# Performance work log

Hardware: AMD Instinct MI355X
Metric: run time of the kernel (lower is better)

## Reference

```python
import jax, jax.numpy as jnp
import numpy as np

B, S_SRC, D, H, DH, FF, L, V, W, NG = 2, 4093, 768, 12, 64, 3072, 2, 50265, 256, 3
S = S_SRC + NG            # 4096, multiple of one-sided window W=256
NC = S // W               # 16 chunks
EPS = 1e-5
CLS_IDS = (50261, 50262, 50263)
NEG = -1e9


def setup_inputs() -> dict:
    key = jax.random.key(0)
    ks = jax.random.split(key, 16)
    std = 0.02
    inp = {
        "src": jax.random.randint(ks[0], (B, S_SRC), 0, 50260),
        "mask_src": jnp.ones((B, S_SRC), dtype=bool),
        "cluster_sizes": jax.random.randint(ks[1], (B,), 0, 16),
        "word_emb": jax.random.normal(ks[2], (V, D), jnp.float32) * std,
        "pos_emb": jax.random.normal(ks[3], (S, D), jnp.float32) * std,
        "emb_ln": jnp.stack([jnp.ones((D,)), jnp.zeros((D,))]),              # [2,D] scale,bias
        "attn_w": jax.random.normal(ks[4], (L, 7, D, D), jnp.float32) * std,  # q,k,v,qg,kg,vg,o
        "attn_b": jnp.zeros((L, 7, D), jnp.float32),
        "ln_p": jnp.stack([jnp.stack([jnp.ones((D,)), jnp.zeros((D,)), jnp.ones((D,)), jnp.zeros((D,))]) for _ in range(L)]),  # [L,4,D]
        "ffn_w1": jax.random.normal(ks[5], (L, D, FF), jnp.float32) * std,
        "ffn_b1": jnp.zeros((L, FF), jnp.float32),
        "ffn_w2": jax.random.normal(ks[6], (L, FF, D), jnp.float32) * std,
        "ffn_b2": jnp.zeros((L, D), jnp.float32),
        "cls_w": jax.random.normal(ks[7], (3, D), jnp.float32) * std,
        "cls_b": jnp.zeros((3,), jnp.float32),
    }
    return inp


def _ln(x, scale, bias):
    mu = jnp.mean(x, axis=-1, keepdims=True)
    var = jnp.mean(jnp.square(x - mu), axis=-1, keepdims=True)
    return (x - mu) * jax.lax.rsqrt(var + EPS) * scale + bias


def _encoder(ids, mask, word_emb, pos_emb, emb_ln, attn_w, attn_b, ln_p,
             ffn_w1, ffn_b1, ffn_w2, ffn_b2):
    x = _ln(word_emb[ids] + pos_emb[None, :S], emb_ln[0], emb_ln[1])  # [B,S,D]

    # static banded-attention index structure (chunk of W queries sees 3W keys)
    idx = np.arange(NC)[:, None] * W + np.arange(3 * W)[None, :]  # into padded seq
    kp = idx - W                                                   # absolute key pos
    valid = (kp >= 0) & (kp < S)
    kpc = jnp.asarray(np.clip(kp, 0, S - 1))
    qpos = np.arange(W)[:, None]
    band = jnp.asarray(np.abs(np.arange(3 * W)[None, :] - W - qpos) <= W)  # [W,3W]
    # global & padding keys removed from windowed attention (HF semantics)
    keymask = mask[:, kpc] & jnp.asarray(valid)[None] & jnp.asarray(kp >= NG)[None]  # [B,NC,3W]
    allowed = band[None, None] & keymask[:, :, None, :]  # [B,NC,W,3W]
    scale = 1.0 / np.sqrt(DH)

    def layer(x, p):
        aw, ab, lnp, w1, b1, w2, b2 = p
        def proj(i):
            return (x @ aw[i] + ab[i]).reshape(B, S, H, DH).transpose(0, 2, 1, 3)
        q = proj(0) * scale
        k = proj(1)
        v = proj(2)
        kpad = jnp.pad(k, ((0, 0), (0, 0), (W, W), (0, 0)))
        vpad = jnp.pad(v, ((0, 0), (0, 0), (W, W), (0, 0)))
        Kc = kpad[:, :, kpc + W]  # [B,H,NC,3W,DH] (kpc+W indexes padded)
        Vc = vpad[:, :, kpc + W]
        qc = q.reshape(B, H, NC, W, DH)
        s_loc = jnp.einsum('bhcqd,bhckd->bhcqk', qc, Kc)
        s_loc = jnp.where(allowed[:, None], s_loc, NEG)
        s_glb = jnp.einsum('bhcqd,bhgd->bhcqg', qc, k[:, :, :NG])  # all tokens -> global keys
        probs = jax.nn.softmax(jnp.concatenate([s_glb, s_loc], axis=-1), axis=-1)
        out = (jnp.einsum('bhcqg,bhgd->bhcqd', probs[..., :NG], v[:, :, :NG])
               + jnp.einsum('bhcqk,bhckd->bhcqd', probs[..., NG:], Vc))
        out = out.reshape(B, H, S, DH)
        # global query rows: full attention with global q/k/v projections
        qg = ((x[:, :NG] @ aw[3] + ab[3]).reshape(B, NG, H, DH)) * scale
        kg = (x @ aw[4] + ab[4]).reshape(B, S, H, DH)
        vg = (x @ aw[5] + ab[5]).reshape(B, S, H, DH)
        sg = jnp.einsum('bghd,bshd->bhgs', qg, kg)
        sg = jnp.where(mask[:, None, None, :], sg, NEG)
        og = jnp.einsum('bhgs,bshd->bhgd', jax.nn.softmax(sg, axis=-1), vg)
        out = out.at[:, :, :NG, :].set(og)
        out = out.transpose(0, 2, 1, 3).reshape(B, S, D)
        xa = _ln(x + out @ aw[6] + ab[6], lnp[0], lnp[1])
        h = jax.nn.gelu(xa @ w1 + b1, approximate=False)
        return _ln(xa + h @ w2 + b2, lnp[2], lnp[3]), None

    x, _ = jax.lax.scan(layer, x, (attn_w, attn_b, ln_p, ffn_w1, ffn_b1, ffn_w2, ffn_b2))
    return x


def reference(src, mask_src, cluster_sizes, word_emb, pos_emb, emb_ln, attn_w,
              attn_b, ln_p, ffn_w1, ffn_b1, ffn_w2, ffn_b2, cls_w, cls_b):
    ids = jnp.concatenate([jnp.broadcast_to(jnp.asarray(CLS_IDS), (B, NG)), src], axis=1)
    mask = jnp.concatenate([jnp.ones((B, NG), dtype=bool), mask_src], axis=1)
    h = _encoder(ids, mask, word_emb, pos_emb, emb_ln, attn_w, attn_b, ln_p,
                 ffn_w1, ffn_b1, ffn_w2, ffn_b2)  # [B,S,D]
    mf = mask.astype(h.dtype)
    scores = [jax.nn.sigmoid(h[:, i] @ cls_w[i] + cls_b[i]) * mf[:, i] for i in range(3)]
    verd, pros, cons = (s[:, None] for s in scores)
    return verd, pros, cons, mf[:, 0][:, None]
```

## Files before the change

### kernel.cpp

```cpp
#include <hip/hip_runtime.h>
#include <hip/hip_bf16.h>
#include <math.h>

#define B_    2
#define SSRC_ 4093
#define D_    768
#define H_    12
#define DH_   64
#define FF_   3072
#define NG_   3
#define W_    256
#define S_    4096
#define NC_   16
#define NSPLIT_ 16
#define QB_   128

typedef __attribute__((ext_vector_type(8))) short frag_ab;
typedef __attribute__((ext_vector_type(4))) float f32x4;

#define GL16(gp, lp) __builtin_amdgcn_global_load_lds( \
    (const __attribute__((address_space(1))) void*)(gp), \
    (__attribute__((address_space(3))) void*)(lp), 16, 0, 0)

__device__ __forceinline__ float bflo(unsigned int w) {
    union { float f; unsigned int i; } c; c.i = w << 16; return c.f;
}
__device__ __forceinline__ float bfhi(unsigned int w) {
    union { float f; unsigned int i; } c; c.i = w & 0xffff0000u; return c.f;
}
__device__ __forceinline__ void unp8(uint4 t, float* o) {
    o[0] = bflo(t.x); o[1] = bfhi(t.x); o[2] = bflo(t.y); o[3] = bfhi(t.y);
    o[4] = bflo(t.z); o[5] = bfhi(t.z); o[6] = bflo(t.w); o[7] = bfhi(t.w);
}
__device__ __forceinline__ unsigned short f2bfu(float x) {
    __hip_bfloat16 h = __float2bfloat16(x);
    return *reinterpret_cast<unsigned short*>(&h);
}

__device__ __forceinline__ float block_sum(float v, float* red) {
    int tid = threadIdx.x;
    red[tid] = v;
    __syncthreads();
#pragma unroll
    for (int off = 128; off >= 1; off >>= 1) {
        if (tid < off) red[tid] += red[tid + off];
        __syncthreads();
    }
    float r = red[0];
    __syncthreads();
    return r;
}

__device__ __forceinline__ float block_max(float v, float* red) {
    int tid = threadIdx.x;
    red[tid] = v;
    __syncthreads();
#pragma unroll
    for (int off = 128; off >= 1; off >>= 1) {
        if (tid < off) red[tid] = fmaxf(red[tid], red[tid + off]);
        __syncthreads();
    }
    float r = red[0];
    __syncthreads();
    return r;
}

__device__ __forceinline__ void storeO(float* p, float v) { *p = v; }
__device__ __forceinline__ void storeO(__hip_bfloat16* p, float v) { *p = __float2bfloat16(v); }

__global__ __launch_bounds__(256) void embed_ln_k(
    const int* __restrict__ src, const float* __restrict__ we,
    const float* __restrict__ pe, const float* __restrict__ gam,
    const float* __restrict__ bet, float* __restrict__ X,
    __hip_bfloat16* __restrict__ Xb) {
    __shared__ float red[256];
    int row = blockIdx.x;
    int b = row >> 12;
    int s = row & (S_ - 1);
    int tid = threadIdx.x;
    int id = (s < NG_) ? (50261 + s) : src[b * SSRC_ + (s - NG_)];
    const float* wr = we + (size_t)id * D_;
    const float* pr = pe + (size_t)s * D_;
    float v[3];
    float lsum = 0.f;
#pragma unroll
    for (int j = 0; j < 3; ++j) {
        int c = tid + j * 256;
        v[j] = wr[c] + pr[c];
        lsum += v[j];
    }
    float mu = block_sum(lsum, red) * (1.0f / 768.0f);
    float ls2 = 0.f;
#pragma unroll
    for (int j = 0; j < 3; ++j) { float d = v[j] - mu; ls2 += d * d; }
    float var = block_sum(ls2, red) * (1.0f / 768.0f);
    float rs = rsqrtf(var + 1e-5f);
    float* xr = X + (size_t)row * D_;
    __hip_bfloat16* xbr = Xb + (size_t)row * D_;
#pragma unroll
    for (int j = 0; j < 3; ++j) {
        int c = tid + j * 256;
        float o = (v[j] - mu) * rs * gam[c] + bet[c];
        xr[c] = o;
        xbr[c] = __float2bfloat16(o);
    }
}

__global__ __launch_bounds__(256) void residual_ln_k(
    const float* __restrict__ x, const float* __restrict__ y,
    const float* __restrict__ y2, const float* __restrict__ gam,
    const float* __restrict__ bet, float* __restrict__ out,
    __hip_bfloat16* __restrict__ outb) {
    __shared__ float red[256];
    int row = blockIdx.x;
    int tid = threadIdx.x;
    const float* xr = x + (size_t)row * D_;
    const float* yr = y + (size_t)row * D_;
    const float* y2r = y2 ? y2 + (size_t)row * D_ : nullptr;
    float v[3];
    float lsum = 0.f;
#pragma unroll
    for (int j = 0; j < 3; ++j) {
        int c = tid + j * 256;
        v[j] = xr[c] + yr[c];
        if (y2r) v[j] += y2r[c];
        lsum += v[j];
    }
    float mu = block_sum(lsum, red) * (1.0f / 768.0f);
    float ls2 = 0.f;
#pragma unroll
    for (int j = 0; j < 3; ++j) { float d = v[j] - mu; ls2 += d * d; }
    float var = block_sum(ls2, red) * (1.0f / 768.0f);
    float rs = rsqrtf(var + 1e-5f);
    float* orow = out + (size_t)row * D_;
    __hip_bfloat16* obr = outb ? outb + (size_t)row * D_ : nullptr;
#pragma unroll
    for (int j = 0; j < 3; ++j) {
        int c = tid + j * 256;
        float o = (v[j] - mu) * rs * gam[c] + bet[c];
        orow[c] = o;
        if (obr) obr[c] = __float2bfloat16(o);
    }
}

__global__ __launch_bounds__(256) void convt_k(
    const float* __restrict__ W, __hip_bfloat16* __restrict__ WT,
    int K, int N, int npb ) {
    __shared__ float tile[32][33];
    int mat = blockIdx.x / npb;
    int bx = blockIdx.x - mat * npb;
    int by = blockIdx.y;
    const float* Wm = W + (size_t)mat * K * N;
    __hip_bfloat16* WTm = WT + (size_t)mat * N * K;
    int tx = threadIdx.x & 31, ty = threadIdx.x >> 5;
#pragma unroll
    for (int i = 0; i < 32; i += 8)
        tile[ty + i][tx] = Wm[(size_t)(by * 32 + ty + i) * N + bx * 32 + tx];
    __syncthreads();
#pragma unroll
    for (int i = 0; i < 32; i += 8)
        WTm[(size_t)(bx * 32 + ty + i) * K + by * 32 + tx] = __float2bfloat16(tile[tx][ty + i]);
}

__global__ void pack_bias_k(const float* __restrict__ ab, float* __restrict__ dst) {
    int j = blockIdx.x * 256 + threadIdx.x;
    if (j >= 5 * 768) return;
    int mat = j / 768, c = j - mat * 768;
    int i = (mat < 3) ? mat : mat + 1;
    dst[j] = ab[i * 768 + c];
}

template <int EPI, int SPLIT>
__global__ __launch_bounds__(256) void mfma_gemm_k(
    const __hip_bfloat16* __restrict__ A, const __hip_bfloat16* __restrict__ BT,
    const float* __restrict__ bias, void* __restrict__ Cout,
    int M, int N, int K, size_t matstride) {
    __shared__ __align__(16) __hip_bfloat16 As[4096];
    __shared__ __align__(16) __hip_bfloat16 Bs[4096];
    int tid = threadIdx.x;
    int lane = tid & 63;
    int w = tid >> 6, wr = w >> 1, wc = w & 1;
    int brow = blockIdx.y * 128, bcol = blockIdx.x * 128;
    int z = blockIdx.z, nz = gridDim.z;
    int Kz = K / nz;
    int r0 = tid >> 2, k0 = (tid & 3) * 8;
    const __hip_bfloat16* Ag0 = A + (size_t)(brow + r0) * K + z * Kz + k0;
    const __hip_bfloat16* Ag1 = Ag0 + (size_t)64 * K;
    const __hip_bfloat16* Bg0 = BT + (size_t)(bcol + r0) * K + z * Kz + k0;
    const __hip_bfloat16* Bg1 = Bg0 + (size_t)64 * K;
    __hip_bfloat16* lA0 = &As[tid * 8];
    __hip_bfloat16* lA1 = &As[tid * 8 + 2048];
    __hip_bfloat16* lB0 = &Bs[tid * 8];
    __hip_bfloat16* lB1 = &Bs[tid * 8 + 2048];

    f32x4 acc[4][4];
#pragma unroll
    for (int m = 0; m < 4; ++m)
#pragma unroll
        for (int n = 0; n < 4; ++n) acc[m][n] = (f32x4){0.f, 0.f, 0.f, 0.f};

    int l15 = lane & 15, kb = lane >> 4;
    int aoff = (wr * 64 + l15) * 32 + kb * 8;
    int boff = (wc * 64 + l15) * 32 + kb * 8;

    for (int kt = 0; kt < Kz; kt += 32) {
        GL16(Ag0 + kt, lA0);
        GL16(Ag1 + kt, lA1);
        GL16(Bg0 + kt, lB0);
        GL16(Bg1 + kt, lB1);
        __syncthreads();
        frag_ab af[4], bf[4];
#pragma unroll
        for (int m = 0; m < 4; ++m) af[m] = *(const frag_ab*)&As[aoff + m * 512];
#pragma unroll
        for (int n = 0; n < 4; ++n) bf[n] = *(const frag_ab*)&Bs[boff + n * 512];
        __builtin_amdgcn_s_setprio(1);
#pragma unroll
        for (int m = 0; m < 4; ++m)
#pragma unroll
            for (int n = 0; n < 4; ++n)
                acc[m][n] = __builtin_amdgcn_mfma_f32_16x16x32_bf16(af[m], bf[n], acc[m][n], 0, 0, 0);
        __builtin_amdgcn_s_setprio(0);
        __syncthreads();
    }

    size_t zoff = (size_t)z * M * N;
#pragma unroll
    for (int m = 0; m < 4; ++m) {
        int rowb = brow + wr * 64 + m * 16 + (lane >> 4) * 4;
#pragma unroll
        for (int n = 0; n < 4; ++n) {
            int col = bcol + wc * 64 + n * 16 + l15;
            float bv = (z == 0) ? bias[col] : 0.f;
#pragma unroll
            for (int r = 0; r < 4; ++r) {
                float v = acc[m][n][r] + bv;
                size_t idx;
                if (SPLIT) {
                    int mat = col / 768;
                    idx = (size_t)mat * matstride + (size_t)(rowb + r) * 768 + (col - mat * 768);
                } else {
                    idx = zoff + (size_t)(rowb + r) * N + col;
                }
                if (EPI == 0) {
                    ((float*)Cout)[idx] = v;
                } else if (EPI == 1) {
                    ((__hip_bfloat16*)Cout)[idx] = __float2bfloat16(v);
                } else {
                    float g = 0.5f * v * (1.0f + erff(v * 0.70710678118654752f));
                    ((__hip_bfloat16*)Cout)[idx] = __float2bfloat16(g);
                }
            }
        }
    }
}

__global__ __launch_bounds__(256) void skinny_gemm_k(
    const float* __restrict__ A, const float* __restrict__ W,
    float* __restrict__ partial, int N, int K) {
    __shared__ float Asl[6][64];
    __shared__ float red[4][6][64];
    int tid = threadIdx.x;
    int cl = tid & 63;
    int kg = tid >> 6;
    int col = blockIdx.x * 64 + cl;
    int k0 = blockIdx.y * 64;
    for (int i = tid; i < 6 * 64; i += 256)
        Asl[i >> 6][i & 63] = A[(size_t)(i >> 6) * K + k0 + (i & 63)];
    __syncthreads();
    float acc[6] = {0.f, 0.f, 0.f, 0.f, 0.f, 0.f};
#pragma unroll
    for (int kk = 0; kk < 16; ++kk) {
        int k = kg * 16 + kk;
        float wv = W[(size_t)(k0 + k) * N + col];
#pragma unroll
        for (int m = 0; m < 6; ++m) acc[m] += Asl[m][k] * wv;
    }
#pragma unroll
    for (int m = 0; m < 6; ++m) red[kg][m][cl] = acc[m];
    __syncthreads();
    for (int i = tid; i < 6 * 64; i += 256) {
        int m = i >> 6, lane = i & 63;
        float s = red[0][m][lane] + red[1][m][lane] + red[2][m][lane] + red[3][m][lane];
        partial[(size_t)blockIdx.y * 6 * N + (size_t)m * N + blockIdx.x * 64 + lane] = s;
    }
}

__global__ __launch_bounds__(256) void skinny_reduce_k(
    const float* __restrict__ partial, const float* __restrict__ bias,
    float* __restrict__ outp, int N, int KS, int gelu) {
    int idx = blockIdx.x * 256 + threadIdx.x;
    if (idx >= 6 * N) return;
    int m = idx / N, col = idx - m * N;
    float s = bias[col];
    for (int kb = 0; kb < KS; ++kb)
        s += partial[(size_t)kb * 6 * N + (size_t)m * N + col];
    if (gelu) s = 0.5f * s * (1.0f + erff(s * 0.70710678118654752f));
    outp[(size_t)m * N + col] = s;
}

__global__ __launch_bounds__(256, 1) void local_attn_k(
    const __hip_bfloat16* __restrict__ Q, const __hip_bfloat16* __restrict__ K,
    const __hip_bfloat16* __restrict__ V, __hip_bfloat16* __restrict__ O) {
    __shared__ __align__(16) __hip_bfloat16 K_lds[64 * 72];
    __shared__ __align__(16) __hip_bfloat16 VT_lds[64 * 72];
    __shared__ __align__(16) __hip_bfloat16 P_lds[4][16 * 72];

    const int cq = blockIdx.x, h = blockIdx.y, b = blockIdx.z;
    const int tid = threadIdx.x;
    const int lane = tid & 63;
    const int w = tid >> 6;
    const int l15 = lane & 15, g4 = lane >> 4;
    const int cbase = cq * QB_;

    frag_ab qf[2][2];
#pragma unroll
    for (int qt = 0; qt < 2; ++qt) {
        int qa = cbase + w * 32 + qt * 16 + l15;
        const __hip_bfloat16* qp = Q + (size_t)(b * S_ + qa) * D_ + h * DH_ + g4 * 8;
        qf[qt][0] = *(const frag_ab*)qp;
        qf[qt][1] = *(const frag_ab*)(qp + 32);
    }

    f32x4 o[2][4];
#pragma unroll
    for (int qt = 0; qt < 2; ++qt)
#pragma unroll
        for (int dt = 0; dt < 4; ++dt) o[qt][dt] = (f32x4){0.f, 0.f, 0.f, 0.f};
    float mrun[2] = {-1e30f, -1e30f};
    float lrun[2] = {0.f, 0.f};

    int kw0 = cbase - W_; if (kw0 < 0) kw0 = 0;
    int kw1 = cbase + QB_ + W_; if (kw1 > S_) kw1 = S_;
    int ntiles = (kw1 - kw0) >> 6;

    char* Pw = (char*)P_lds[w];

    for (int t = 0; t < ntiles; ++t) {
        int k0 = kw0 + t * 64;
        __syncthreads();
        {
            const __hip_bfloat16* Kg = K + (size_t)(b * S_ + k0) * D_ + h * DH_;
            const __hip_bfloat16* Vg = V + (size_t)(b * S_ + k0) * D_ + h * DH_;
#pragma unroll
            for (int it = 0; it < 2; ++it) {
                int idx = tid + it * 256;
                int kk = idx >> 3, d0 = (idx & 7) * 8;
                uint4 kv = *(const uint4*)(Kg + (size_t)kk * D_ + d0);
                *(uint4*)&K_lds[kk * 72 + d0] = kv;
                uint4 vv = *(const uint4*)(Vg + (size_t)kk * D_ + d0);
                unsigned short vs[8];
                *(uint4*)vs = vv;
#pragma unroll
                for (int j = 0; j < 8; ++j) {
                    int dd = d0 + j;
                    int boff = dd * 144 + ((kk * 2) ^ (((dd >> 3) & 7) << 4));
                    *(unsigned short*)((char*)VT_lds + boff) = vs[j];
                }
            }
        }
        __syncthreads();

        frag_ab kf[4][2];
#pragma unroll
        for (int kt = 0; kt < 4; ++kt) {
            const char* kp = (const char*)K_lds + (kt * 16 + l15) * 144 + g4 * 16;
            kf[kt][0] = *(const frag_ab*)kp;
            kf[kt][1] = *(const frag_ab*)(kp + 64);
        }
        frag_ab vf[4][2];
#pragma unroll
        for (int dt = 0; dt < 4; ++dt) {
            int drow = dt * 16 + l15;
            int swz = ((drow >> 3) & 7) << 4;
            const char* vp = (const char*)VT_lds + drow * 144;
            vf[dt][0] = *(const frag_ab*)(vp + ((g4 * 16) ^ swz));
            vf[dt][1] = *(const frag_ab*)(vp + ((g4 * 16 + 64) ^ swz));
        }

#pragma unroll
        for (int qt = 0; qt < 2; ++qt) {
            f32x4 st[4];
            __builtin_amdgcn_s_setprio(1);
#pragma unroll
            for (int kt = 0; kt < 4; ++kt) {
                f32x4 z = (f32x4){0.f, 0.f, 0.f, 0.f};
                z = __builtin_amdgcn_mfma_f32_16x16x32_bf16(kf[kt][0], qf[qt][0], z, 0, 0, 0);
                z = __builtin_amdgcn_mfma_f32_16x16x32_bf16(kf[kt][1], qf[qt][1], z, 0, 0, 0);
                st[kt] = z;
            }
            __builtin_amdgcn_s_setprio(0);
            int qa = cbase + w * 32 + qt * 16 + l15;
            float sv[16];
            float mx = -1e30f;
#pragma unroll
            for (int kt = 0; kt < 4; ++kt)
#pragma unroll
                for (int r = 0; r < 4; ++r) {
                    int ka = k0 + kt * 16 + g4 * 4 + r;
                    float s = st[kt][r] * 0.125f;
                    bool bad = (ka < NG_) | (ka - qa > W_) | (qa - ka > W_);
                    s = bad ? -1e30f : s;
                    sv[kt * 4 + r] = s;
                    mx = fmaxf(mx, s);
                }
            mx = fmaxf(mx, __shfl_xor(mx, 16));
            mx = fmaxf(mx, __shfl_xor(mx, 32));
            float mnew = fmaxf(fmaxf(mrun[qt], mx), -60.0f);
            if (__any(mnew != mrun[qt])) {
                float fsc = __expf(mrun[qt] - mnew);
                mrun[qt] = mnew;
#pragma unroll
                for (int dt = 0; dt < 4; ++dt) o[qt][dt] *= fsc;
                lrun[qt] *= fsc;
            }
            float psum = 0.f;
            unsigned short pb[16];
#pragma unroll
            for (int i = 0; i < 16; ++i) {
                float p = __expf(sv[i] - mrun[qt]);
                psum += p;
                pb[i] = f2bfu(p);
            }
            psum += __shfl_xor(psum, 16);
            psum += __shfl_xor(psum, 32);
            lrun[qt] += psum;
#pragma unroll
            for (int kt = 0; kt < 4; ++kt)
#pragma unroll
                for (int rp = 0; rp < 2; ++rp) {
                    unsigned vpk = (unsigned)pb[kt * 4 + rp * 2] | ((unsigned)pb[kt * 4 + rp * 2 + 1] << 16);
                    int kloc = kt * 16 + g4 * 4 + rp * 2;
                    *(unsigned*)(Pw + l15 * 144 + kloc * 2) = vpk;
                }
            frag_ab pf0 = *(const frag_ab*)(Pw + l15 * 144 + g4 * 16);
            frag_ab pf1 = *(const frag_ab*)(Pw + l15 * 144 + g4 * 16 + 64);
            __builtin_amdgcn_s_setprio(1);
#pragma unroll
            for (int dt = 0; dt < 4; ++dt) {
                o[qt][dt] = __builtin_amdgcn_mfma_f32_16x16x32_bf16(vf[dt][0], pf0, o[qt][dt], 0, 0, 0);
                o[qt][dt] = __builtin_amdgcn_mfma_f32_16x16x32_bf16(vf[dt][1], pf1, o[qt][dt], 0, 0, 0);
            }
            __builtin_amdgcn_s_setprio(0);
        }
    }

    uint4 kgc[3][2];
    uint2 vgd[3][4];
#pragma unroll
    for (int gk = 0; gk < NG_; ++gk) {
        const __hip_bfloat16* kp = K + (size_t)(b * S_ + gk) * D_ + h * DH_ + g4 * 8;
        kgc[gk][0] = *(const uint4*)kp;
        kgc[gk][1] = *(const uint4*)(kp + 32);
        const __hip_bfloat16* vp = V + (size_t)(b * S_ + gk) * D_ + h * DH_ + g4 * 4;
#pragma unroll
        for (int dt = 0; dt < 4; ++dt)
            vgd[gk][dt] = *(const uint2*)(vp + dt * 16);
    }
#pragma unroll
    for (int qt = 0; qt < 2; ++qt) {
        float sg[3];
#pragma unroll
        for (int gk = 0; gk < NG_; ++gk) {
            float part = 0.f;
#pragma unroll
            for (int s = 0; s < 2; ++s) {
                uint4 qw = *(uint4*)&qf[qt][s];
                uint4 kw = kgc[gk][s];
                part += bflo(qw.x) * bflo(kw.x) + bfhi(qw.x) * bfhi(kw.x);
                part += bflo(qw.y) * bflo(kw.y) + bfhi(qw.y) * bfhi(kw.y);
                part += bflo(qw.z) * bflo(kw.z) + bfhi(qw.z) * bfhi(kw.z);
                part += bflo(qw.w) * bflo(kw.w) + bfhi(qw.w) * bfhi(kw.w);
            }
            part += __shfl_xor(part, 16);
            part += __shfl_xor(part, 32);
            sg[gk] = part * 0.125f;
        }
        float mx3 = fmaxf(fmaxf(sg[0], sg[1]), sg[2]);
        float mnew = fmaxf(fmaxf(mrun[qt], mx3), -60.0f);
        float fsc = __expf(mrun[qt] - mnew);
        mrun[qt] = mnew;
#pragma unroll
        for (int dt = 0; dt < 4; ++dt) o[qt][dt] *= fsc;
        lrun[qt] *= fsc;
        float pg[3];
        float psum = 0.f;
#pragma unroll
        for (int gk = 0; gk < NG_; ++gk) { pg[gk] = __expf(sg[gk] - mnew); psum += pg[gk]; }
        lrun[qt] += psum;
#pragma unroll
        for (int dt = 0; dt < 4; ++dt) {
#pragma unroll
            for (int gk = 0; gk < NG_; ++gk) {
                uint2 vv = vgd[gk][dt];
                o[qt][dt][0] += pg[gk] * bflo(vv.x);
                o[qt][dt][1] += pg[gk] * bfhi(vv.x);
                o[qt][dt][2] += pg[gk] * bflo(vv.y);
                o[qt][dt][3] += pg[gk] * bfhi(vv.y);
            }
        }
    }

#pragma unroll
    for (int qt = 0; qt < 2; ++qt) {
        float linv = 1.0f / lrun[qt];
        int qa = cbase + w * 32 + qt * 16 + l15;
        __hip_bfloat16* orow = O + (size_t)(b * S_ + qa) * D_ + h * DH_;
#pragma unroll
        for (int dt = 0; dt < 4; ++dt) {
            unsigned short pk[4];
#pragma unroll
            for (int r = 0; r < 4; ++r) pk[r] = f2bfu(o[qt][dt][r] * linv);
            *(uint2*)(orow + dt * 16 + g4 * 4) = *(uint2*)pk;
        }
    }
}

__global__ __launch_bounds__(256) void gattn_part_k(
    const float* __restrict__ qg, const __hip_bfloat16* __restrict__ KG,
    const __hip_bfloat16* __restrict__ VG, float* __restrict__ gpart) {
    __shared__ float sc[256];
    __shared__ float qs[DH_];
    __shared__ float red[256];
    __shared__ float rv[16][64];
    int split = blockIdx.x;
    int gh = blockIdx.y;
    int g = gh / H_, h = gh - g * H_;
    int b = blockIdx.z;
    int tid = threadIdx.x;
    if (tid < DH_) qs[tid] = qg[(size_t)(b * NG_ + g) * D_ + h * DH_ + tid] * 0.125f;
    __syncthreads();
    int s0 = split * (S_ / NSPLIT_);
    float acc = 0.f;
    {
        const __hip_bfloat16* kp = KG + (size_t)(b * S_ + s0 + tid) * D_ + h * DH_;
#pragma unroll
        for (int c8 = 0; c8 < 8; ++c8) {
            uint4 t = *(const uint4*)(kp + c8 * 8);
            float f[8]; unp8(t, f);
#pragma unroll
            for (int j = 0; j < 8; ++j) acc += qs[c8 * 8 + j] * f[j];
        }
    }
    float m = block_max(acc, red);
    float e = __expf(acc - m);
    sc[tid] = e;
    float l = block_sum(e, red);
    int sgq = tid >> 4, dq = (tid & 15) * 4;
    float a0 = 0.f, a1 = 0.f, a2 = 0.f, a3 = 0.f;
    const __hip_bfloat16* vbase = VG + (size_t)(b * S_ + s0 + sgq * 16) * D_ + h * DH_ + dq;
#pragma unroll
    for (int i = 0; i < 16; ++i) {
        float p = sc[sgq * 16 + i];
        uint2 vv = *(const uint2*)(vbase + (size_t)i * D_);
        a0 += p * bflo(vv.x); a1 += p * bfhi(vv.x);
        a2 += p * bflo(vv.y); a3 += p * bfhi(vv.y);
    }
    rv[sgq][dq] = a0; rv[sgq][dq + 1] = a1; rv[sgq][dq + 2] = a2; rv[sgq][dq + 3] = a3;
    __syncthreads();
    float* op = gpart + ((size_t)((b * NG_ + g) * H_ + h) * NSPLIT_ + split) * 66;
    if (tid == 0) { op[0] = m; op[1] = l; }
    if (tid < DH_) {
        float s = 0.f;
#pragma unroll
        for (int j = 0; j < 16; ++j) s += rv[j][tid];
        op[2 + tid] = s;
    }
}

template <typename TO>
__global__ __launch_bounds__(64) void gattn_comb_k(
    const float* __restrict__ gpart, TO* __restrict__ outp, int rowStride) {
    int g = blockIdx.x, h = blockIdx.y, b = blockIdx.z;
    int tid = threadIdx.x;
    const float* base = gpart + (size_t)((b * NG_ + g) * H_ + h) * NSPLIT_ * 66;
    float M = -1e30f;
#pragma unroll
    for (int p = 0; p < NSPLIT_; ++p) M = fmaxf(M, base[p * 66]);
    float l = 0.f, o = 0.f;
#pragma unroll
    for (int p = 0; p < NSPLIT_; ++p) {
        float wgt = __expf(base[p * 66] - M);
        l += wgt * base[p * 66 + 1];
        o += wgt * base[p * 66 + 2 + tid];
    }
    storeO(&outp[(size_t)(b * rowStride + g) * D_ + h * DH_ + tid], o / l);
}

__global__ void gather6_k(const float* __restrict__ X, float* __restrict__ xg) {
    int r = blockIdx.x;
    int b = r / NG_, g = r % NG_;
    for (int c = threadIdx.x; c < D_; c += blockDim.x)
        xg[(size_t)r * D_ + c] = X[(size_t)(b * S_ + g) * D_ + c];
}

__global__ __launch_bounds__(256) void classifier_k(
    const float* __restrict__ x26, const float* __restrict__ cw,
    const float* __restrict__ cb, float* __restrict__ out) {
    __shared__ float red[256];
    int tid = threadIdx.x;
    for (int i = 0; i < 3; ++i) {
        for (int b = 0; b < B_; ++b) {
            const float* xr = x26 + (size_t)(b * NG_ + i) * D_;
            const float* wr = cw + (size_t)i * D_;
            float p = 0.f;
            for (int c = tid; c < D_; c += 256) p += xr[c] * wr[c];
            float dotv = block_sum(p, red);
            if (tid == 0) out[i * B_ + b] = 1.0f / (1.0f + __expf(-(dotv + cb[i])));
        }
    }
    if (tid == 0) { out[6] = 1.0f; out[7] = 1.0f; }
}

extern "C" void kernel_launch(void* const* d_in, const int* in_sizes, int n_in,
                              void* d_out, int out_size, void* d_ws, size_t ws_size,
                              hipStream_t stream) {
    const int*   src      = (const int*)d_in[0];
    const float* word_emb = (const float*)d_in[3];
    const float* pos_emb  = (const float*)d_in[4];
    const float* emb_ln   = (const float*)d_in[5];
    const float* attn_w   = (const float*)d_in[6];
    const float* attn_b   = (const float*)d_in[7];
    const float* ln_p     = (const float*)d_in[8];
    const float* ffn_w1   = (const float*)d_in[9];
    const float* ffn_b1   = (const float*)d_in[10];
    const float* ffn_w2   = (const float*)d_in[11];
    const float* ffn_b2   = (const float*)d_in[12];
    const float* cls_w    = (const float*)d_in[13];
    const float* cls_b    = (const float*)d_in[14];
    float* out = (float*)d_out;

    const size_t NT = (size_t)B_ * S_ * D_;
    float* base = (float*)d_ws;
    float* X  = base;
    float* P4 = base + NT;
    __hip_bfloat16* Xb  = (__hip_bfloat16*)(base + 2 * NT);
    __hip_bfloat16* Qb  = (__hip_bfloat16*)(base + 5 * NT / 2);
    __hip_bfloat16* Kb  = (__hip_bfloat16*)(base + 3 * NT);
    __hip_bfloat16* Vb  = (__hip_bfloat16*)(base + 7 * NT / 2);
    __hip_bfloat16* KGb = (__hip_bfloat16*)(base + 4 * NT);
    __hip_bfloat16* VGb = (__hip_bfloat16*)(base + 9 * NT / 2);
    __hip_bfloat16* AOb = (__hip_bfloat16*)(base + 5 * NT);
    __hip_bfloat16* HCb = (__hip_bfloat16*)(base + 11 * NT / 2);
    float* pj1 = base + 15 * NT / 2;
    float* pj2 = base + 17 * NT / 2;
    __hip_bfloat16* wq5 = (__hip_bfloat16*)(base + 19 * NT / 2);
    __hip_bfloat16* wo  = wq5 + 5 * 589824;
    __hip_bfloat16* wg1 = wo + 589824;
    __hip_bfloat16* wf1 = wg1 + 2 * 589824;
    __hip_bfloat16* wf2 = wf1 + 2359296;
    float* SM  = (float*)(wf2 + 2359296);
    float* xg  = SM;
    float* qg6 = xg + 6 * D_;
    float* og6 = qg6 + 6 * D_;
    float* pr6 = og6 + 6 * D_;
    float* xa6 = pr6 + 6 * D_;
    float* h6  = xa6 + 6 * D_;
    float* f6  = h6 + 6 * FF_;
    float* x26 = f6 + 6 * D_;
    float* bias5 = x26 + 6 * D_;
    float* part = bias5 + 5 * D_;
    float* gpart = part;

    const int M = B_ * S_;
    dim3 blk(256);

    auto aw = [&](int l, int i) { return attn_w + ((size_t)(l * 7 + i)) * D_ * D_; };
    auto ab = [&](int l, int i) { return attn_b + (size_t)(l * 7 + i) * D_; };
    auto lnp = [&](int l, int i) { return ln_p + (size_t)(l * 4 + i) * D_; };

    auto skinny = [&](const float* A6, const float* Wm, const float* bias,
                      float* out6, int N, int K, int gelu) {
        skinny_gemm_k<<<dim3(N / 64, K / 64), blk, 0, stream>>>(A6, Wm, part, N, K);
        skinny_reduce_k<<<dim3((6 * N + 255) / 256), blk, 0, stream>>>(part, bias, out6, N, K / 64, gelu);
    };

    embed_ln_k<<<M, blk, 0, stream>>>(src, word_emb, pos_emb, emb_ln, emb_ln + D_, X, Xb);

    convt_k<<<dim3(24 * 3, 24), blk, 0, stream>>>(aw(0, 0), wq5, D_, D_, 24);
    convt_k<<<dim3(24 * 2, 24), blk, 0, stream>>>(aw(0, 4), wq5 + 3 * 589824, D_, D_, 24);
    pack_bias_k<<<15, blk, 0, stream>>>(ab(0, 0), bias5);
    mfma_gemm_k<1, 1><<<dim3(3840 / 128, 64), blk, 0, stream>>>(Xb, wq5, bias5, Qb, M, 3840, D_, NT);
    local_attn_k<<<dim3(S_ / QB_, H_, B_), blk, 0, stream>>>(Qb, Kb, Vb, AOb);
    gather6_k<<<B_ * NG_, blk, 0, stream>>>(X, xg);
    skinny(xg, aw(0, 3), ab(0, 3), qg6, D_, D_, 0);
    gattn_part_k<<<dim3(NSPLIT_, NG_ * H_, B_), blk, 0, stream>>>(qg6, KGb, VGb, gpart);
    gattn_comb_k<__hip_bfloat16><<<dim3(NG_, H_, B_), dim3(64), 0, stream>>>(gpart, AOb, S_);
    convt_k<<<dim3(24, 24), blk, 0, stream>>>(aw(0, 6), wo, D_, D_, 24);
    mfma_gemm_k<0, 0><<<dim3(6, 64, 2), blk, 0, stream>>>(AOb, wo, ab(0, 6), pj1, M, D_, D_, 0);
    residual_ln_k<<<M, blk, 0, stream>>>(X, pj1, pj2, lnp(0, 0), lnp(0, 1), P4, Xb);
    convt_k<<<dim3(96, 24), blk, 0, stream>>>(ffn_w1, wf1, D_, FF_, 96);
    convt_k<<<dim3(24, 96), blk, 0, stream>>>(ffn_w2, wf2, FF_, D_, 24);
    mfma_gemm_k<2, 0><<<dim3(24, 64), blk, 0, stream>>>(Xb, wf1, ffn_b1, HCb, M, FF_, D_, 0);
    mfma_gemm_k<0, 0><<<dim3(6, 64, 2), blk, 0, stream>>>(HCb, wf2, ffn_b2, pj1, M, D_, FF_, 0);
    residual_ln_k<<<M, blk, 0, stream>>>(P4, pj1, pj2, lnp(0, 2), lnp(0, 3), X, Xb);

    convt_k<<<dim3(24 * 2, 24), blk, 0, stream>>>(aw(1, 4), wg1, D_, D_, 24);
    mfma_gemm_k<1, 1><<<dim3(1536 / 128, 64), blk, 0, stream>>>(Xb, wg1, ab(1, 4), KGb, M, 1536, D_, NT);
    gather6_k<<<B_ * NG_, blk, 0, stream>>>(X, xg);
    skinny(xg, aw(1, 3), ab(1, 3), qg6, D_, D_, 0);
    gattn_part_k<<<dim3(NSPLIT_, NG_ * H_, B_), blk, 0, stream>>>(qg6, KGb, VGb, gpart);
    gattn_comb_k<float><<<dim3(NG_, H_, B_), dim3(64), 0, stream>>>(gpart, og6, NG_);
    skinny(og6, aw(1, 6), ab(1, 6), pr6, D_, D_, 0);
    residual_ln_k<<<B_ * NG_, blk, 0, stream>>>(xg, pr6, nullptr, lnp(1, 0), lnp(1, 1), xa6, nullptr);
    skinny(xa6, ffn_w1 + (size_t)D_ * FF_, ffn_b1 + FF_, h6, FF_, D_, 1);
    skinny(h6, ffn_w2 + (size_t)FF_ * D_, ffn_b2 + D_, f6, D_, FF_, 0);
    residual_ln_k<<<B_ * NG_, blk, 0, stream>>>(xa6, f6, nullptr, lnp(1, 2), lnp(1, 3), x26, nullptr);
    classifier_k<<<1, blk, 0, stream>>>(x26, cls_w, cls_b, out);
}
```

Before: 516.8 us.

## Double-buffer LDS tiles in MFMA GEMM and remap blocks per XCD

The bf16 MFMA GEMM now keeps two LDS buffers for the A and B tiles. It issues the global_load_lds for the next K-tile before computing on the current one, so memory latency overlaps with MFMA work instead of being serialized behind a barrier. It also remaps the workgroup id so blocks dispatched round-robin across the 8 XCDs get contiguous output tiles, which should improve L2 reuse of A and B panels. LDS use per block doubles, which could lower occupancy. The correctness of the prefetch depends on the end-of-loop barrier waiting for the async loads.

```diff
diff --git a/kernel.cpp b/kernel.cpp
--- a/kernel.cpp
+++ b/kernel.cpp
@@ -175,12 +175,19 @@
     const __hip_bfloat16* __restrict__ A, const __hip_bfloat16* __restrict__ BT,
     const float* __restrict__ bias, void* __restrict__ Cout,
     int M, int N, int K, size_t matstride) {
-    __shared__ __align__(16) __hip_bfloat16 As[4096];
-    __shared__ __align__(16) __hip_bfloat16 Bs[4096];
+    __shared__ __align__(16) __hip_bfloat16 As[2][4096];
+    __shared__ __align__(16) __hip_bfloat16 Bs[2][4096];
     int tid = threadIdx.x;
     int lane = tid & 63;
     int w = tid >> 6, wr = w >> 1, wc = w & 1;
-    int brow = blockIdx.y * 128, bcol = blockIdx.x * 128;
+    int nwg = gridDim.x * gridDim.y;
+    int id = blockIdx.y * gridDim.x + blockIdx.x;
+    if ((nwg & 7) == 0) {
+        int per = nwg >> 3;
+        id = (id & 7) * per + (id >> 3);
+    }
+    int bx = id % gridDim.x, by = id / gridDim.x;
+    int brow = by * 128, bcol = bx * 128;
     int z = blockIdx.z, nz = gridDim.z;
     int Kz = K / nz;
     int r0 = tid >> 2, k0 = (tid & 3) * 8;
@@ -188,10 +195,6 @@
     const __hip_bfloat16* Ag1 = Ag0 + (size_t)64 * K;
     const __hip_bfloat16* Bg0 = BT + (size_t)(bcol + r0) * K + z * Kz + k0;
     const __hip_bfloat16* Bg1 = Bg0 + (size_t)64 * K;
-    __hip_bfloat16* lA0 = &As[tid * 8];
-    __hip_bfloat16* lA1 = &As[tid * 8 + 2048];
-    __hip_bfloat16* lB0 = &Bs[tid * 8];
-    __hip_bfloat16* lB1 = &Bs[tid * 8 + 2048];
 
     f32x4 acc[4][4];
 #pragma unroll
@@ -203,17 +206,28 @@
     int aoff = (wr * 64 + l15) * 32 + kb * 8;
     int boff = (wc * 64 + l15) * 32 + kb * 8;
 
-    for (int kt = 0; kt < Kz; kt += 32) {
-        GL16(Ag0 + kt, lA0);
-        GL16(Ag1 + kt, lA1);
-        GL16(Bg0 + kt, lB0);
-        GL16(Bg1 + kt, lB1);
-        __syncthreads();
+    int nt = Kz >> 5;
+    GL16(Ag0, &As[0][tid * 8]);
+    GL16(Ag1, &As[0][tid * 8 + 2048]);
+    GL16(Bg0, &Bs[0][tid * 8]);
+    GL16(Bg1, &Bs[0][tid * 8 + 2048]);
+    __syncthreads();
+
+    for (int t = 0; t < nt; ++t) {
+        int cur = t & 1;
+        if (t + 1 < nt) {
+            int nxt = cur ^ 1;
+            int kt = (t + 1) << 5;
+            GL16(Ag0 + kt, &As[nxt][tid * 8]);
+            GL16(Ag1 + kt, &As[nxt][tid * 8 + 2048]);
+            GL16(Bg0 + kt, &Bs[nxt][tid * 8]);
+            GL16(Bg1 + kt, &Bs[nxt][tid * 8 + 2048]);
+        }
         frag_ab af[4], bf[4];
 #pragma unroll
-        for (int m = 0; m < 4; ++m) af[m] = *(const frag_ab*)&As[aoff + m * 512];
-#pragma unroll
-        for (int n = 0; n < 4; ++n) bf[n] = *(const frag_ab*)&Bs[boff + n * 512];
+        for (int m = 0; m < 4; ++m) af[m] = *(const frag_ab*)&As[cur][aoff + m * 512];
+#pragma unroll
+        for (int n = 0; n < 4; ++n) bf[n] = *(const frag_ab*)&Bs[cur][boff + n * 512];
         __builtin_amdgcn_s_setprio(1);
 #pragma unroll
         for (int m = 0; m < 4; ++m)
```

Measured after the change: 504.9 us, median of 2. 1.02x faster.
